# Kernel optimization log

Measured on AMD Instinct MI355X. Metric: run time of the kernel, lower is better.

## Reference

```python
import jax, jax.numpy as jnp
import numpy as np

B, N, D = 16, 2048, 128
SCALE = 1.0 / np.sqrt(D).astype(np.float32)


def setup_inputs() -> dict:
    key = jax.random.key(0)
    ks = jax.random.split(key, 9)
    Q = jax.random.normal(ks[0], (B, N, D), dtype=jnp.float32)
    K = jax.random.normal(ks[1], (B, N, D), dtype=jnp.float32)
    V = jax.random.normal(ks[2], (B, N, D), dtype=jnp.float32)
    bias_dis = 0.1 * jax.random.normal(ks[3], (N, N), dtype=jnp.float32)
    bias_dtw = 0.1 * jax.random.normal(ks[4], (N, N), dtype=jnp.float32)
    bias_pattern = 0.1 * jax.random.normal(ks[5], (N, N), dtype=jnp.float32)
    bias_poi = 0.1 * jax.random.normal(ks[6], (N, N), dtype=jnp.float32)
    # key/query padding masks: mostly True (valid) with some padding
    input_mask = jax.random.randint(ks[7], (B, N), 0, 10) > 0
    embeddings_mask = jax.random.randint(ks[8], (B, N), 0, 10) > 0
    # lower-triangular causal mask (diagonal kept so every row has a valid key)
    causal_mask = jnp.tril(jnp.ones((N, N), dtype=bool))
    return {"Q": Q, "K": K, "V": V, "bias_dis": bias_dis, "bias_dtw": bias_dtw,
            "bias_pattern": bias_pattern, "bias_poi": bias_poi,
            "input_mask": input_mask, "embeddings_mask": embeddings_mask,
            "causal_mask": causal_mask}


def reference(Q, K, V, bias_dis, bias_dtw, bias_pattern, bias_poi,
              input_mask, embeddings_mask, causal_mask):
    # masked_fill_(~mask, 0.0) on K, V with input_mask[:, :, None]
    km = input_mask[:, :, None]
    K = jnp.where(km, K, 0.0)
    V = jnp.where(km, V, 0.0)
    # masked_fill_(~mask, 0.0) on Q with embeddings_mask[:, :, None]
    Q = jnp.where(embeddings_mask[:, :, None], Q, 0.0)
    # scores [B, N, N] = Q K^T / sqrt(dim)
    scores = jnp.einsum('bnd,bmd->bnm', Q, K) * SCALE
    # causal masked_fill_(~causal_mask, -inf)
    scores = jnp.where(causal_mask[None, :, :], scores, -jnp.inf)
    # per-batch bias loop == broadcast add of summed [N, N] biases
    scores = scores + (bias_dis + bias_dtw + bias_pattern + bias_poi)[None, :, :]
    P = jax.nn.softmax(scores, axis=-1)
    # dropout p=0 (eval) -> identity
    return jnp.einsum('bnm,bmd->bnd', P, V)
```

## Files before the change

kernel.cpp:

```cpp
#include <hip/hip_runtime.h>
#include <math.h>

constexpr int Bc = 16;
constexpr int Nc = 2048;
constexpr int Dc = 128;
constexpr int NCHUNK = Nc / 64;
constexpr float SCALE_F = 0.08838834764831845f;

typedef __bf16 bf16x8 __attribute__((ext_vector_type(8)));
typedef __bf16 bf16x4 __attribute__((ext_vector_type(4)));
typedef float  f32x4  __attribute__((ext_vector_type(4)));

constexpr size_t KPACK_BYTES = (size_t)Bc * NCHUNK * 16 * 64 * 16;
constexpr size_t VPACK_BYTES = KPACK_BYTES;
constexpr int NUNITS = 1056;
constexpr size_t BIASP_BYTES = (size_t)NUNITS * 2048 * 4;
constexpr int CHUNK_ELEMS = 16 * 64 * 8;
constexpr int PART_FLOATS = 64 * 128 + 64 + 64;
constexpr size_t PART_BYTES = (size_t)Bc * 72 * PART_FLOATS * 4;

__device__ __constant__ int SLOT_UNITS[32][3] = {
    { 7,  6,  1}, { 8, 21, 11}, {10, 44, 29}, {12, 75, 55},
    {14,  5,  2}, {16, 19, 13}, {18, 41, 32}, {20, 71, 59},
    {22,  4,  3}, {23, 17, 15}, {24, 38, 35}, {25, 67, 63},
    {27, 28,  0}, {30, 31,  9}, {33, 34, 26}, {36, 37, 51},
    {39, 40, -1}, {42, 43, -1}, {45, 46, -1}, {47, 48, -1},
    {49, 50, -1}, {52, 53, -1}, {54, 56, -1}, {57, 58, -1},
    {60, 61, -1}, {62, 64, -1}, {65, 66, -1}, {68, 69, -1},
    {70, 72, -1}, {73, 74, -1}, {76, 77, -1}, {78, 79, -1}
};

__device__ __forceinline__ int ftri(int t) {
    const int m = t >> 1;
    return (t & 1) ? (m + 1) * (m + 1) : m * (m + 1);
}

__device__ __forceinline__ void gload_lds16(const __bf16* gsrc, __bf16* ldst) {
    __builtin_amdgcn_global_load_lds(
        (const __attribute__((address_space(1))) unsigned int*)gsrc,
        (__attribute__((address_space(3))) unsigned int*)ldst, 16, 0, 0);
}

template<int CTRL>
__device__ __forceinline__ float dpp_mv(float v) {
    return __builtin_bit_cast(float,
        __builtin_amdgcn_update_dpp(0, __builtin_bit_cast(int, v),
                                    CTRL, 0xF, 0xF, true));
}
__device__ __forceinline__ float rmax16(float v) {
    v = fmaxf(v, dpp_mv<0xB1>(v));
    v = fmaxf(v, dpp_mv<0x4E>(v));
    v = fmaxf(v, dpp_mv<0x141>(v));
    v = fmaxf(v, dpp_mv<0x140>(v));
    return v;
}
__device__ __forceinline__ float rsum16(float v) {
    v += dpp_mv<0xB1>(v);
    v += dpp_mv<0x4E>(v);
    v += dpp_mv<0x141>(v);
    v += dpp_mv<0x140>(v);
    return v;
}

__global__ __launch_bounds__(256) void prep_fused(
    const float* __restrict__ K, const float* __restrict__ V,
    const int* __restrict__ imask,
    const float* __restrict__ b0, const float* __restrict__ b1,
    const float* __restrict__ b2, const float* __restrict__ b3,
    __bf16* __restrict__ Kp, __bf16* __restrict__ Vp, float* __restrict__ bsp)
{
    __shared__ __align__(16) __bf16 Ks[64][136];
    __shared__ __align__(16) __bf16 Vs[64][136];
    __shared__ __align__(16) float  Ts[32][68];
    const int bid = blockIdx.x;
    const int tid = threadIdx.x;

    if (bid >= 512) {
        const int u = bid - 512;
        int t = 0;
        while (ftri(t + 1) <= u) ++t;
        const int c = u - ftri(t);

        #pragma unroll
        for (int i = 0; i < 2; ++i) {
            const int v = tid + 256 * i;
            const int row = v >> 4, c4 = v & 15;
            const size_t g = (size_t)(t * 32 + row) * Nc + c * 64 + c4 * 4;
            const float4 a = *(const float4*)(b0 + g);
            const float4 d = *(const float4*)(b1 + g);
            const float4 e = *(const float4*)(b2 + g);
            const float4 f = *(const float4*)(b3 + g);
            float4 s;
            s.x = a.x + d.x + e.x + f.x;
            s.y = a.y + d.y + e.y + f.y;
            s.z = a.z + d.z + e.z + f.z;
            s.w = a.w + d.w + e.w + f.w;
            *(float4*)&Ts[row][c4 * 4] = s;
        }
        __syncthreads();

        const int lane = tid >> 2;
        const int quad = lane >> 4, l15 = lane & 15;
        const int k0 = (tid & 3) * 8;
        float* outp = bsp + (size_t)u * 2048;
        #pragma unroll
        for (int g2 = 0; g2 < 2; ++g2) {
            const int k = k0 + g2 * 4;
            const int h = (k >> 4) & 1, jt = (k >> 2) & 3;
            float4 o;
            o.x = Ts[h * 16 + quad * 4 + 0][jt * 16 + l15];
            o.y = Ts[h * 16 + quad * 4 + 1][jt * 16 + l15];
            o.z = Ts[h * 16 + quad * 4 + 2][jt * 16 + l15];
            o.w = Ts[h * 16 + quad * 4 + 3][jt * 16 + l15];
            ((float4*)outp)[tid * 2 + g2] = o;
        }
        return;
    }

    const int c = bid & 31;
    const int b = bid >> 5;
    const int m0 = c * 64;
    const float* Kb = K + (size_t)b * Nc * Dc;
    const float* Vb = V + (size_t)b * Nc * Dc;
    const int* imb = imask + b * Nc;

    #pragma unroll
    for (int it = 0; it < 8; ++it) {
        const int idx = it * 256 + tid;
        const int row = idx >> 5;
        const int c4  = idx & 31;
        const int gm  = m0 + row;
        const float msk = imb[gm] ? 1.0f : 0.0f;
        const float4 kf = ((const float4*)(Kb + (size_t)gm * Dc))[c4];
        const float4 vf = ((const float4*)(Vb + (size_t)gm * Dc))[c4];
        bf16x4 kb, vb;
        kb[0] = (__bf16)(kf.x * msk); kb[1] = (__bf16)(kf.y * msk);
        kb[2] = (__bf16)(kf.z * msk); kb[3] = (__bf16)(kf.w * msk);
        vb[0] = (__bf16)(vf.x * msk); vb[1] = (__bf16)(vf.y * msk);
        vb[2] = (__bf16)(vf.z * msk); vb[3] = (__bf16)(vf.w * msk);
        *(bf16x4*)&Ks[row][c4 * 4] = kb;
        *(bf16x4*)&Vs[row][c4 * 4] = vb;
    }
    __syncthreads();

    const size_t chunk_base = (size_t)(b * NCHUNK + c) * CHUNK_ELEMS;
    #pragma unroll
    for (int i = 0; i < 4; ++i) {
        const int s = i * 256 + tid;
        const int f = s >> 6;
        const int l = s & 63;
        const int quad = (l >> 4) & 3;
        const int l15  = l & 15;
        {
            const int jt = f >> 2, kd = f & 3;
            const bf16x8 kv = *(const bf16x8*)&Ks[jt * 16 + l15][kd * 32 + quad * 8];
            *(bf16x8*)&Kp[chunk_base + (size_t)f * 512 + l * 8] = kv;
        }
        {
            const int kj = f >> 3, dt = f & 7;
            bf16x8 vv;
            #pragma unroll
            for (int j = 0; j < 8; ++j)
                vv[j] = Vs[kj * 32 + quad * 8 + j][dt * 16 + l15];
            *(bf16x8*)&Vp[chunk_base + (size_t)f * 512 + l * 8] = vv;
        }
    }
}

template<bool SPLIT>
__global__ __launch_bounds__(256) void attn_persist(
    const float* __restrict__ Q,
    const __bf16* __restrict__ Kp, const __bf16* __restrict__ Vp,
    const float* __restrict__ biasp, const int* __restrict__ emask,
    float* __restrict__ out, float* __restrict__ part)
{
    __shared__ __align__(16) __bf16 Kl[2][16 * 512];
    __shared__ __align__(16) __bf16 Vl[2][16 * 512];
    __shared__ __align__(16) __bf16 Pl[4][16][72];

    const int tid  = threadIdx.x;
    const int w    = tid >> 6;
    const int lane = tid & 63;
    const int quad = lane >> 4;
    const int l15  = lane & 15;
    const int b    = blockIdx.x;
    const int slot = blockIdx.y;

    const float*  Qb  = Q + (size_t)b * Nc * Dc;
    const __bf16* Kpb = Kp + (size_t)b * NCHUNK * CHUNK_ELEMS;
    const __bf16* Vpb = Vp + (size_t)b * NCHUNK * CHUNK_ELEMS;
    const f32x4* bfragbase = (const f32x4*)biasp + (size_t)lane * 8 + (w & 1) * 4;

    for (int j = 0; j < 3; ++j) {
        int t, c0, cend, pidx;
        bool direct;
        if (SPLIT) {
            const int un = SLOT_UNITS[slot][j];
            if (un < 0) break;
            if (un < 8)       { t = un;                  c0 = 0; }
            else if (un < 24) { t = 8  + ((un -  8) >> 1); c0 = ((un -  8) & 1) * 8; }
            else if (un < 48) { t = 16 + (un - 24) / 3;    c0 = ((un - 24) % 3) * 8; }
            else              { t = 24 + ((un - 48) >> 2); c0 = ((un - 48) & 3) * 8; }
            cend = min(t + 1, c0 + 8);
            direct = (un < 8);
            pidx = un - 8;
        } else {
            if (j) break;
            t = (slot < 16) ? slot : (47 - slot);
            c0 = 0; cend = t + 1; direct = true; pidx = 0;
        }

        const int q0w = t * 64 + w * 16;
        const int t32 = t * 2 + (w >> 1);
        const int fb32 = ftri(t32);
        const f32x4* bfrag = bfragbase;

        bf16x8 qfrag[4];
        {
            const int row = q0w + l15;
            const float qs = emask[b * Nc + row] ? SCALE_F : 0.0f;
            const float4* qr = (const float4*)(Qb + (size_t)row * Dc);
            #pragma unroll
            for (int kd = 0; kd < 4; ++kd) {
                const float4 xx = qr[kd * 8 + quad * 2];
                const float4 yy = qr[kd * 8 + quad * 2 + 1];
                qfrag[kd][0] = (__bf16)(xx.x * qs); qfrag[kd][1] = (__bf16)(xx.y * qs);
                qfrag[kd][2] = (__bf16)(xx.z * qs); qfrag[kd][3] = (__bf16)(xx.w * qs);
                qfrag[kd][4] = (__bf16)(yy.x * qs); qfrag[kd][5] = (__bf16)(yy.y * qs);
                qfrag[kd][6] = (__bf16)(yy.z * qs); qfrag[kd][7] = (__bf16)(yy.w * qs);
            }
        }

        f32x4 oacc[8];
        #pragma unroll
        for (int dt = 0; dt < 8; ++dt) { oacc[dt][0]=0.f; oacc[dt][1]=0.f; oacc[dt][2]=0.f; oacc[dt][3]=0.f; }
        float mrun[4] = {-INFINITY, -INFINITY, -INFINITY, -INFINITY};
        float lrun[4] = {0.f, 0.f, 0.f, 0.f};

        const int nch = cend - c0;

        #pragma unroll
        for (int i = 0; i < 4; ++i) {
            const int seg = w * 4 + i;
            gload_lds16(Kpb + (size_t)c0 * CHUNK_ELEMS + seg * 512 + lane * 8, &Kl[0][seg * 512]);
            gload_lds16(Vpb + (size_t)c0 * CHUNK_ELEMS + seg * 512 + lane * 8, &Vl[0][seg * 512]);
        }
        f32x4 binit[4];
        #pragma unroll
        for (int jt = 0; jt < 4; ++jt)
            binit[jt] = bfrag[(size_t)(fb32 + c0) * 512 + jt];
        __syncthreads();

        f32x4 sc[4];
        #pragma unroll
        for (int jt = 0; jt < 4; ++jt) sc[jt] = binit[jt];
        #pragma unroll
        for (int jt = 0; jt < 4; ++jt)
            #pragma unroll
            for (int kd = 0; kd < 4; ++kd) {
                const bf16x8 bfr = *(const bf16x8*)&Kl[0][(jt * 4 + kd) * 512 + lane * 8];
                sc[jt] = __builtin_amdgcn_mfma_f32_16x16x32_bf16(qfrag[kd], bfr, sc[jt], 0, 0, 0);
            }
        if (nch > 1) {
            #pragma unroll
            for (int i = 0; i < 4; ++i) {
                const int seg = w * 4 + i;
                gload_lds16(Kpb + (size_t)(c0 + 1) * CHUNK_ELEMS + seg * 512 + lane * 8, &Kl[1][seg * 512]);
                gload_lds16(Vpb + (size_t)(c0 + 1) * CHUNK_ELEMS + seg * 512 + lane * 8, &Vl[1][seg * 512]);
            }
            #pragma unroll
            for (int jt = 0; jt < 4; ++jt)
                binit[jt] = bfrag[(size_t)(fb32 + c0 + 1) * 512 + jt];
        }

        for (int c = c0; c < cend; ++c) {
            const int cb = (c - c0) & 1;

            if (c == t) {
                const int m0 = c * 64;
                #pragma unroll
                for (int jt = 0; jt < 4; ++jt)
                    #pragma unroll
                    for (int reg = 0; reg < 4; ++reg) {
                        const int gr = q0w + quad * 4 + reg;
                        const int gc = m0 + jt * 16 + l15;
                        if (gc > gr) sc[jt][reg] = -INFINITY;
                    }
            }

            float mx[4];
            int grow = 0;
            #pragma unroll
            for (int reg = 0; reg < 4; ++reg) {
                float m = fmaxf(fmaxf(sc[0][reg], sc[1][reg]), fmaxf(sc[2][reg], sc[3][reg]));
                m = rmax16(m);
                mx[reg] = m;
                grow |= (m > mrun[reg]);
            }
            if (__any(grow)) {
                #pragma unroll
                for (int reg = 0; reg < 4; ++reg) {
                    const float mn = fmaxf(mrun[reg], mx[reg]);
                    const float alpha = __expf(mrun[reg] - mn);
                    mrun[reg] = mn;
                    lrun[reg] *= alpha;
                    #pragma unroll
                    for (int dt = 0; dt < 8; ++dt) oacc[dt][reg] *= alpha;
                }
            }
            #pragma unroll
            for (int reg = 0; reg < 4; ++reg) {
                float ls = 0.f;
                #pragma unroll
                for (int jt = 0; jt < 4; ++jt) {
                    const float pv = __expf(sc[jt][reg] - mrun[reg]);
                    sc[jt][reg] = pv;
                    ls += pv;
                }
                lrun[reg] += rsum16(ls);
            }

            #pragma unroll
            for (int jt = 0; jt < 4; ++jt)
                #pragma unroll
                for (int reg = 0; reg < 4; ++reg)
                    Pl[w][quad * 4 + reg][jt * 16 + l15] = (__bf16)sc[jt][reg];

            #pragma unroll
            for (int kj = 0; kj < 2; ++kj) {
                const bf16x8 pa = *(const bf16x8*)&Pl[w][l15][kj * 32 + quad * 8];
                #pragma unroll
                for (int dt = 0; dt < 8; ++dt) {
                    const bf16x8 vb = *(const bf16x8*)&Vl[cb][(kj * 8 + dt) * 512 + lane * 8];
                    oacc[dt] = __builtin_amdgcn_mfma_f32_16x16x32_bf16(pa, vb, oacc[dt], 0, 0, 0);
                }
            }

            __syncthreads();

            const bool n1 = (c + 1) < cend;
            const bool n2 = (c + 2) < cend;

            if (n2) {
                const size_t off = (size_t)(c + 2) * CHUNK_ELEMS;
                #pragma unroll
                for (int i = 0; i < 4; ++i) {
                    const int seg = w * 4 + i;
                    gload_lds16(Kpb + off + seg * 512 + lane * 8, &Kl[cb][seg * 512]);
                    gload_lds16(Vpb + off + seg * 512 + lane * 8, &Vl[cb][seg * 512]);
                }
            }

            if (n1) {
                #pragma unroll
                for (int jt = 0; jt < 4; ++jt) sc[jt] = binit[jt];
                #pragma unroll
                for (int jt = 0; jt < 4; ++jt)
                    #pragma unroll
                    for (int kd = 0; kd < 4; ++kd) {
                        const bf16x8 bfr = *(const bf16x8*)&Kl[cb ^ 1][(jt * 4 + kd) * 512 + lane * 8];
                        sc[jt] = __builtin_amdgcn_mfma_f32_16x16x32_bf16(qfrag[kd], bfr, sc[jt], 0, 0, 0);
                    }
            }
            if (n2) {
                #pragma unroll
                for (int jt = 0; jt < 4; ++jt)
                    binit[jt] = bfrag[(size_t)(fb32 + c + 2) * 512 + jt];
            }
        }

        if (direct) {
            #pragma unroll
            for (int reg = 0; reg < 4; ++reg) {
                const float inv = 1.0f / lrun[reg];
                const int gr = q0w + quad * 4 + reg;
                float* orow = out + ((size_t)b * Nc + gr) * Dc;
                #pragma unroll
                for (int dt = 0; dt < 8; ++dt)
                    orow[dt * 16 + l15] = oacc[dt][reg] * inv;
            }
        } else {
            float* pb = part + (size_t)(b * 72 + pidx) * PART_FLOATS;
            #pragma unroll
            for (int reg = 0; reg < 4; ++reg) {
                const int lr = w * 16 + quad * 4 + reg;
                #pragma unroll
                for (int dt = 0; dt < 8; ++dt)
                    pb[lr * 128 + dt * 16 + l15] = oacc[dt][reg];
                if (l15 == 0) {
                    pb[8192 + lr] = mrun[reg];
                    pb[8256 + lr] = lrun[reg];
                }
            }
        }
    }
}

__global__ __launch_bounds__(256) void merge_parts(
    const float* __restrict__ part, float* __restrict__ out)
{
    const int b = blockIdx.x;
    const int t = 8 + blockIdx.y;
    const int S = (t < 16) ? 2 : ((t < 24) ? 3 : 4);
    const int pbase = (t < 16) ? 2 * (t - 8)
                    : (t < 24) ? 16 + 3 * (t - 16)
                               : 40 + 4 * (t - 24);
    const int r  = threadIdx.x >> 2;
    const int cq = threadIdx.x & 3;
    const float* p0 = part + (size_t)(b * 72 + pbase) * PART_FLOATS;

    float m[4], a[4];
    float mstar = -INFINITY;
    #pragma unroll
    for (int s = 0; s < 4; ++s)
        if (s < S) { m[s] = p0[(size_t)s * PART_FLOATS + 8192 + r]; mstar = fmaxf(mstar, m[s]); }
    float lsum = 0.f;
    #pragma unroll
    for (int s = 0; s < 4; ++s)
        if (s < S) {
            a[s] = __expf(m[s] - mstar);
            lsum += p0[(size_t)s * PART_FLOATS + 8256 + r] * a[s];
        }
    const float inv = 1.0f / lsum;

    float* orow = out + ((size_t)b * Nc + t * 64 + r) * Dc + cq * 32;
    #pragma unroll
    for (int i = 0; i < 8; ++i) {
        float x = 0.f, y = 0.f, z = 0.f, ww = 0.f;
        #pragma unroll
        for (int s = 0; s < 4; ++s)
            if (s < S) {
                const f32x4 v = *(const f32x4*)&p0[(size_t)s * PART_FLOATS + r * 128 + cq * 32 + i * 4];
                x += v[0] * a[s]; y += v[1] * a[s]; z += v[2] * a[s]; ww += v[3] * a[s];
            }
        f32x4 o; o[0] = x * inv; o[1] = y * inv; o[2] = z * inv; o[3] = ww * inv;
        *(f32x4*)&orow[i * 4] = o;
    }
}

__global__ __launch_bounds__(256) void attn_mfma_legacy(
    const float* __restrict__ Q, const float* __restrict__ K, const float* __restrict__ V,
    const float* __restrict__ p0, const float* __restrict__ p1,
    const float* __restrict__ p2, const float* __restrict__ p3,
    const int* __restrict__ imask, const int* __restrict__ emask,
    float* __restrict__ out)
{
    __shared__ __align__(16) __bf16 Klds[64][136];
    __shared__ __align__(16) __bf16 Vt[128][72];
    __shared__ __align__(16) __bf16 Plds[4][16][72];
    const int tid  = threadIdx.x;
    const int w    = tid >> 6;
    const int lane = tid & 63;
    const int quad = lane >> 4;
    const int l15  = lane & 15;
    const int b = blockIdx.y;
    const int x = blockIdx.x, yy = blockIdx.y;
    const int ti = (yy < 8) ? x : (31 - x);
    const int q0 = ti * 64, q0w = q0 + w * 16;
    const float* Qb = Q + (size_t)b * Nc * Dc;
    const float* Kb = K + (size_t)b * Nc * Dc;
    const float* Vb = V + (size_t)b * Nc * Dc;
    const int* imb = imask + b * Nc;

    bf16x8 qfrag[4];
    {
        const int row = q0w + l15;
        const float qs = emask[b * Nc + row] ? SCALE_F : 0.0f;
        const float4* qr = (const float4*)(Qb + (size_t)row * Dc);
        #pragma unroll
        for (int kd = 0; kd < 4; ++kd) {
            const float4 xv = qr[kd * 8 + quad * 2];
            const float4 yv = qr[kd * 8 + quad * 2 + 1];
            qfrag[kd][0]=(__bf16)(xv.x*qs); qfrag[kd][1]=(__bf16)(xv.y*qs);
            qfrag[kd][2]=(__bf16)(xv.z*qs); qfrag[kd][3]=(__bf16)(xv.w*qs);
            qfrag[kd][4]=(__bf16)(yv.x*qs); qfrag[kd][5]=(__bf16)(yv.y*qs);
            qfrag[kd][6]=(__bf16)(yv.z*qs); qfrag[kd][7]=(__bf16)(yv.w*qs);
        }
    }
    f32x4 oacc[8];
    #pragma unroll
    for (int dt = 0; dt < 8; ++dt){oacc[dt][0]=0.f;oacc[dt][1]=0.f;oacc[dt][2]=0.f;oacc[dt][3]=0.f;}
    float mrun[4]={-INFINITY,-INFINITY,-INFINITY,-INFINITY}, lrun[4]={0.f,0.f,0.f,0.f};

    for (int m0 = 0; m0 <= q0; m0 += 64) {
        __syncthreads();
        #pragma unroll
        for (int it = 0; it < 8; ++it) {
            const int idx = it * 256 + tid;
            const int row = idx >> 5, c4 = idx & 31;
            const int gm = m0 + row;
            const float msk = imb[gm] ? 1.0f : 0.0f;
            const float4 kf = ((const float4*)(Kb + (size_t)gm * Dc))[c4];
            const float4 vf = ((const float4*)(Vb + (size_t)gm * Dc))[c4];
            bf16x4 kb;
            kb[0]=(__bf16)(kf.x*msk); kb[1]=(__bf16)(kf.y*msk);
            kb[2]=(__bf16)(kf.z*msk); kb[3]=(__bf16)(kf.w*msk);
            *(bf16x4*)&Klds[row][c4*4] = kb;
            Vt[c4*4+0][row]=(__bf16)(vf.x*msk); Vt[c4*4+1][row]=(__bf16)(vf.y*msk);
            Vt[c4*4+2][row]=(__bf16)(vf.z*msk); Vt[c4*4+3][row]=(__bf16)(vf.w*msk);
        }
        __syncthreads();
        f32x4 sc[4];
        #pragma unroll
        for (int jt = 0; jt < 4; ++jt){sc[jt][0]=0.f;sc[jt][1]=0.f;sc[jt][2]=0.f;sc[jt][3]=0.f;}
        #pragma unroll
        for (int jt = 0; jt < 4; ++jt)
            #pragma unroll
            for (int kd = 0; kd < 4; ++kd) {
                const bf16x8 bfr = *(const bf16x8*)&Klds[jt*16+l15][kd*32+quad*8];
                sc[jt] = __builtin_amdgcn_mfma_f32_16x16x32_bf16(qfrag[kd], bfr, sc[jt], 0, 0, 0);
            }
        #pragma unroll
        for (int jt = 0; jt < 4; ++jt)
            #pragma unroll
            for (int reg = 0; reg < 4; ++reg) {
                const int gr = q0w + quad*4 + reg;
                const int gc = m0 + jt*16 + l15;
                const size_t boff = (size_t)gr * Nc + gc;
                const float bsx = p0[boff] + p1[boff] + p2[boff] + p3[boff];
                const float v = sc[jt][reg] + bsx;
                sc[jt][reg] = (gc > gr) ? -INFINITY : v;
            }
        #pragma unroll
        for (int reg = 0; reg < 4; ++reg) {
            float mx = fmaxf(fmaxf(sc[0][reg], sc[1][reg]), fmaxf(sc[2][reg], sc[3][reg]));
            mx = rmax16(mx);
            const float mn = fmaxf(mrun[reg], mx);
            const float alpha = __expf(mrun[reg] - mn);
            mrun[reg] = mn; lrun[reg] *= alpha;
            #pragma unroll
            for (int dt = 0; dt < 8; ++dt) oacc[dt][reg] *= alpha;
            float ls = 0.f;
            #pragma unroll
            for (int jt = 0; jt < 4; ++jt) {
                const float pv = __expf(sc[jt][reg] - mn);
                sc[jt][reg] = pv; ls += pv;
            }
            lrun[reg] += rsum16(ls);
        }
        #pragma unroll
        for (int jt = 0; jt < 4; ++jt)
            #pragma unroll
            for (int reg = 0; reg < 4; ++reg)
                Plds[w][quad*4+reg][jt*16+l15] = (__bf16)sc[jt][reg];
        #pragma unroll
        for (int kj = 0; kj < 2; ++kj) {
            const bf16x8 pa = *(const bf16x8*)&Plds[w][l15][kj*32+quad*8];
            #pragma unroll
            for (int dt = 0; dt < 8; ++dt) {
                const bf16x8 vb = *(const bf16x8*)&Vt[dt*16+l15][kj*32+quad*8];
                oacc[dt] = __builtin_amdgcn_mfma_f32_16x16x32_bf16(pa, vb, oacc[dt], 0, 0, 0);
            }
        }
    }
    #pragma unroll
    for (int reg = 0; reg < 4; ++reg) {
        const float inv = 1.0f / lrun[reg];
        const int gr = q0w + quad*4 + reg;
        float* orow = out + ((size_t)b * Nc + gr) * Dc;
        #pragma unroll
        for (int dt = 0; dt < 8; ++dt)
            orow[dt*16+l15] = oacc[dt][reg] * inv;
    }
}

extern "C" void kernel_launch(void* const* d_in, const int* in_sizes, int n_in,
                              void* d_out, int out_size, void* d_ws, size_t ws_size,
                              hipStream_t stream) {
    const float* Q  = (const float*)d_in[0];
    const float* K  = (const float*)d_in[1];
    const float* V  = (const float*)d_in[2];
    const float* b0 = (const float*)d_in[3];
    const float* b1 = (const float*)d_in[4];
    const float* b2 = (const float*)d_in[5];
    const float* b3 = (const float*)d_in[6];
    const int* im   = (const int*)d_in[7];
    const int* em   = (const int*)d_in[8];
    float* out      = (float*)d_out;

    const size_t need_full  = KPACK_BYTES + VPACK_BYTES + BIASP_BYTES;
    const size_t need_split = need_full + PART_BYTES;

    if (ws_size >= need_full) {
        __bf16* Kp  = (__bf16*)d_ws;
        __bf16* Vp  = (__bf16*)((char*)d_ws + KPACK_BYTES);
        float*  bsp = (float*)((char*)d_ws + KPACK_BYTES + VPACK_BYTES);
        float*  prt = (float*)((char*)d_ws + need_full);
        prep_fused<<<512 + NUNITS, 256, 0, stream>>>(
            K, V, im, b0, b1, b2, b3, Kp, Vp, bsp);
        if (ws_size >= need_split) {
            attn_persist<true><<<dim3(Bc, 32), 256, 0, stream>>>(
                Q, Kp, Vp, bsp, em, out, prt);
            merge_parts<<<dim3(Bc, 24), 256, 0, stream>>>(prt, out);
        } else {
            attn_persist<false><<<dim3(Bc, 32), 256, 0, stream>>>(
                Q, Kp, Vp, bsp, em, out, nullptr);
        }
    } else {
        attn_mfma_legacy<<<dim3(NCHUNK, Bc), 256, 0, stream>>>(
            Q, K, V, b0, b1, b2, b3, im, em, out);
    }
}
```

Measured before the change: 234.2 us.

## Load V fragments directly to registers, swizzle P tile, and double slot count

V chunks are now read straight from global memory into registers for the PV matmul, so they are no longer staged through LDS. This halves the shared memory footprint and allows more blocks per CU. The P scratch tile drops its padding in favour of an XOR swizzle to avoid bank conflicts. The split path launches 64 slots per batch with a rebalanced unit-to-slot table, which raises parallelism. The costs are higher register pressure, global V loads whose latency sits in the critical loop, and more partial merges.

```diff
diff --git a/kernel.cpp b/kernel.cpp
--- a/kernel.cpp
+++ b/kernel.cpp
@@ -19,15 +19,23 @@
 constexpr int PART_FLOATS = 64 * 128 + 64 + 64;
 constexpr size_t PART_BYTES = (size_t)Bc * 72 * PART_FLOATS * 4;
 
-__device__ __constant__ int SLOT_UNITS[32][3] = {
-    { 7,  6,  1}, { 8, 21, 11}, {10, 44, 29}, {12, 75, 55},
-    {14,  5,  2}, {16, 19, 13}, {18, 41, 32}, {20, 71, 59},
-    {22,  4,  3}, {23, 17, 15}, {24, 38, 35}, {25, 67, 63},
-    {27, 28,  0}, {30, 31,  9}, {33, 34, 26}, {36, 37, 51},
-    {39, 40, -1}, {42, 43, -1}, {45, 46, -1}, {47, 48, -1},
-    {49, 50, -1}, {52, 53, -1}, {54, 56, -1}, {57, 58, -1},
-    {60, 61, -1}, {62, 64, -1}, {65, 66, -1}, {68, 69, -1},
-    {70, 72, -1}, {73, 74, -1}, {76, 77, -1}, {78, 79, -1}
+__device__ __constant__ signed char SLOT_UNITS[64][3] = {
+    { 6,  2, -1}, {21, 13, -1}, {44, 32, -1}, {75, 59, -1},
+    { 5,  3, -1}, {19, 15, -1}, {41, 35, -1}, {71, 63, -1},
+    { 4,  1,  0}, {17, 11,  9}, {38, 29, 26}, {67, 55, 51},
+    { 7, -1, -1}, { 8, -1, -1}, {10, -1, -1}, {12, -1, -1},
+    {14, -1, -1}, {16, -1, -1}, {18, -1, -1}, {20, -1, -1},
+    {22, -1, -1}, {23, -1, -1}, {24, -1, -1}, {25, -1, -1},
+    {27, -1, -1}, {28, -1, -1}, {30, -1, -1}, {31, -1, -1},
+    {33, -1, -1}, {34, -1, -1}, {36, -1, -1}, {37, -1, -1},
+    {39, -1, -1}, {40, -1, -1}, {42, -1, -1}, {43, -1, -1},
+    {45, -1, -1}, {46, -1, -1}, {47, -1, -1}, {48, -1, -1},
+    {49, -1, -1}, {50, -1, -1}, {52, -1, -1}, {53, -1, -1},
+    {54, -1, -1}, {56, -1, -1}, {57, -1, -1}, {58, -1, -1},
+    {60, -1, -1}, {61, -1, -1}, {62, -1, -1}, {64, -1, -1},
+    {65, -1, -1}, {66, -1, -1}, {68, -1, -1}, {69, -1, -1},
+    {70, -1, -1}, {72, -1, -1}, {73, -1, -1}, {74, -1, -1},
+    {76, -1, -1}, {77, -1, -1}, {78, -1, -1}, {79, -1, -1}
 };
 
 __device__ __forceinline__ int ftri(int t) {
@@ -39,6 +47,10 @@
     __builtin_amdgcn_global_load_lds(
         (const __attribute__((address_space(1))) unsigned int*)gsrc,
         (__attribute__((address_space(3))) unsigned int*)ldst, 16, 0, 0);
+}
+
+__device__ __forceinline__ int pswz(int row, int col) {
+    return col ^ ((row & 7) << 3);
 }
 
 template<int CTRL>
@@ -168,15 +180,14 @@
 }
 
 template<bool SPLIT>
-__global__ __launch_bounds__(256) void attn_persist(
+__global__ __launch_bounds__(256) void attn_persist2(
     const float* __restrict__ Q,
     const __bf16* __restrict__ Kp, const __bf16* __restrict__ Vp,
     const float* __restrict__ biasp, const int* __restrict__ emask,
     float* __restrict__ out, float* __restrict__ part)
 {
     __shared__ __align__(16) __bf16 Kl[2][16 * 512];
-    __shared__ __align__(16) __bf16 Vl[2][16 * 512];
-    __shared__ __align__(16) __bf16 Pl[4][16][72];
+    __shared__ __align__(16) __bf16 Pl[4][16][64];
 
     const int tid  = threadIdx.x;
     const int w    = tid >> 6;
@@ -243,7 +254,6 @@
         for (int i = 0; i < 4; ++i) {
             const int seg = w * 4 + i;
             gload_lds16(Kpb + (size_t)c0 * CHUNK_ELEMS + seg * 512 + lane * 8, &Kl[0][seg * 512]);
-            gload_lds16(Vpb + (size_t)c0 * CHUNK_ELEMS + seg * 512 + lane * 8, &Vl[0][seg * 512]);
         }
         f32x4 binit[4];
         #pragma unroll
@@ -253,20 +263,20 @@
 
         f32x4 sc[4];
         #pragma unroll
-        for (int jt = 0; jt < 4; ++jt) sc[jt] = binit[jt];
-        #pragma unroll
-        for (int jt = 0; jt < 4; ++jt)
-            #pragma unroll
-            for (int kd = 0; kd < 4; ++kd) {
+        for (int jt = 0; jt < 4; ++jt) {
+            const bf16x8 k0f = *(const bf16x8*)&Kl[0][(jt * 4 + 0) * 512 + lane * 8];
+            sc[jt] = __builtin_amdgcn_mfma_f32_16x16x32_bf16(qfrag[0], k0f, binit[jt], 0, 0, 0);
+            #pragma unroll
+            for (int kd = 1; kd < 4; ++kd) {
                 const bf16x8 bfr = *(const bf16x8*)&Kl[0][(jt * 4 + kd) * 512 + lane * 8];
                 sc[jt] = __builtin_amdgcn_mfma_f32_16x16x32_bf16(qfrag[kd], bfr, sc[jt], 0, 0, 0);
             }
+        }
         if (nch > 1) {
             #pragma unroll
             for (int i = 0; i < 4; ++i) {
                 const int seg = w * 4 + i;
                 gload_lds16(Kpb + (size_t)(c0 + 1) * CHUNK_ELEMS + seg * 512 + lane * 8, &Kl[1][seg * 512]);
-                gload_lds16(Vpb + (size_t)(c0 + 1) * CHUNK_ELEMS + seg * 512 + lane * 8, &Vl[1][seg * 512]);
             }
             #pragma unroll
             for (int jt = 0; jt < 4; ++jt)
@@ -275,6 +285,12 @@
 
         for (int c = c0; c < cend; ++c) {
             const int cb = (c - c0) & 1;
+            const __bf16* vc = Vpb + (size_t)c * CHUNK_ELEMS;
+
+            bf16x8 va[8];
+            #pragma unroll
+            for (int dt = 0; dt < 8; ++dt)
+                va[dt] = *(const bf16x8*)&vc[(size_t)dt * 512 + lane * 8];
 
             if (c == t) {
                 const int m0 = c * 64;
@@ -323,17 +339,25 @@
             #pragma unroll
             for (int jt = 0; jt < 4; ++jt)
                 #pragma unroll
-                for (int reg = 0; reg < 4; ++reg)
-                    Pl[w][quad * 4 + reg][jt * 16 + l15] = (__bf16)sc[jt][reg];
-
-            #pragma unroll
-            for (int kj = 0; kj < 2; ++kj) {
-                const bf16x8 pa = *(const bf16x8*)&Pl[w][l15][kj * 32 + quad * 8];
-                #pragma unroll
-                for (int dt = 0; dt < 8; ++dt) {
-                    const bf16x8 vb = *(const bf16x8*)&Vl[cb][(kj * 8 + dt) * 512 + lane * 8];
-                    oacc[dt] = __builtin_amdgcn_mfma_f32_16x16x32_bf16(pa, vb, oacc[dt], 0, 0, 0);
+                for (int reg = 0; reg < 4; ++reg) {
+                    const int row = quad * 4 + reg;
+                    Pl[w][row][pswz(row, jt * 16 + l15)] = (__bf16)sc[jt][reg];
                 }
+
+            bf16x8 vb8[8];
+            #pragma unroll
+            for (int dt = 0; dt < 8; ++dt)
+                vb8[dt] = *(const bf16x8*)&vc[(size_t)(8 + dt) * 512 + lane * 8];
+
+            {
+                const bf16x8 pa0 = *(const bf16x8*)&Pl[w][l15][pswz(l15, quad * 8)];
+                #pragma unroll
+                for (int dt = 0; dt < 8; ++dt)
+                    oacc[dt] = __builtin_amdgcn_mfma_f32_16x16x32_bf16(pa0, va[dt], oacc[dt], 0, 0, 0);
+                const bf16x8 pa1 = *(const bf16x8*)&Pl[w][l15][pswz(l15, 32 + quad * 8)];
+                #pragma unroll
+                for (int dt = 0; dt < 8; ++dt)
+                    oacc[dt] = __builtin_amdgcn_mfma_f32_16x16x32_bf16(pa1, vb8[dt], oacc[dt], 0, 0, 0);
             }
 
             __syncthreads();
@@ -347,20 +371,20 @@
                 for (int i = 0; i < 4; ++i) {
                     const int seg = w * 4 + i;
                     gload_lds16(Kpb + off + seg * 512 + lane * 8, &Kl[cb][seg * 512]);
-                    gload_lds16(Vpb + off + seg * 512 + lane * 8, &Vl[cb][seg * 512]);
                 }
             }
 
             if (n1) {
                 #pragma unroll
-                for (int jt = 0; jt < 4; ++jt) sc[jt] = binit[jt];
-                #pragma unroll
-                for (int jt = 0; jt < 4; ++jt)
+                for (int jt = 0; jt < 4; ++jt) {
+                    const bf16x8 k0f = *(const bf16x8*)&Kl[cb ^ 1][(jt * 4 + 0) * 512 + lane * 8];
+                    sc[jt] = __builtin_amdgcn_mfma_f32_16x16x32_bf16(qfrag[0], k0f, binit[jt], 0, 0, 0);
                     #pragma unroll
-                    for (int kd = 0; kd < 4; ++kd) {
+                    for (int kd = 1; kd < 4; ++kd) {
                         const bf16x8 bfr = *(const bf16x8*)&Kl[cb ^ 1][(jt * 4 + kd) * 512 + lane * 8];
                         sc[jt] = __builtin_amdgcn_mfma_f32_16x16x32_bf16(qfrag[kd], bfr, sc[jt], 0, 0, 0);
                     }
+                }
             }
             if (n2) {
                 #pragma unroll
@@ -589,11 +613,11 @@
         prep_fused<<<512 + NUNITS, 256, 0, stream>>>(
             K, V, im, b0, b1, b2, b3, Kp, Vp, bsp);
         if (ws_size >= need_split) {
-            attn_persist<true><<<dim3(Bc, 32), 256, 0, stream>>>(
+            attn_persist2<true><<<dim3(Bc, 64), 256, 0, stream>>>(
                 Q, Kp, Vp, bsp, em, out, prt);
             merge_parts<<<dim3(Bc, 24), 256, 0, stream>>>(prt, out);
         } else {
-            attn_persist<false><<<dim3(Bc, 32), 256, 0, stream>>>(
+            attn_persist2<false><<<dim3(Bc, 32), 256, 0, stream>>>(
                 Q, Kp, Vp, bsp, em, out, nullptr);
         }
     } else {
```

Result: slower. 271.5 us (+15.9%).

## Widen attention blocks to 128 query rows with 8 waves and rebalanced split schedule

Applied to the files above, without the earlier changes.

The persistent attention kernel now uses 512-thread blocks covering 128 query rows (8 waves), so each K/V chunk loaded into LDS is shared by twice as many rows. The split-KV work table is rebuilt for 128-row tiles with new per-slot chunk ranges and a matching merge kernel. Two smaller changes ride along: the P buffer in LDS gets an XOR swizzle in place of padding, and the per-row sum reduction moves out of the inner loop to the epilogue. The larger block raises register and LDS pressure per workgroup and changes how load is balanced across CUs.

```diff
diff --git a/kernel.cpp b/kernel.cpp
--- a/kernel.cpp
+++ b/kernel.cpp
@@ -16,18 +16,56 @@
 constexpr int NUNITS = 1056;
 constexpr size_t BIASP_BYTES = (size_t)NUNITS * 2048 * 4;
 constexpr int CHUNK_ELEMS = 16 * 64 * 8;
-constexpr int PART_FLOATS = 64 * 128 + 64 + 64;
-constexpr size_t PART_BYTES = (size_t)Bc * 72 * PART_FLOATS * 4;
-
-__device__ __constant__ int SLOT_UNITS[32][3] = {
-    { 7,  6,  1}, { 8, 21, 11}, {10, 44, 29}, {12, 75, 55},
-    {14,  5,  2}, {16, 19, 13}, {18, 41, 32}, {20, 71, 59},
-    {22,  4,  3}, {23, 17, 15}, {24, 38, 35}, {25, 67, 63},
-    {27, 28,  0}, {30, 31,  9}, {33, 34, 26}, {36, 37, 51},
-    {39, 40, -1}, {42, 43, -1}, {45, 46, -1}, {47, 48, -1},
-    {49, 50, -1}, {52, 53, -1}, {54, 56, -1}, {57, 58, -1},
-    {60, 61, -1}, {62, 64, -1}, {65, 66, -1}, {68, 69, -1},
-    {70, 72, -1}, {73, 74, -1}, {76, 77, -1}, {78, 79, -1}
+constexpr int PART_FLOATS8 = 128 * 128 + 128 + 128;
+constexpr int NPART8 = 42;
+constexpr size_t PART_BYTES8 = (size_t)Bc * NPART8 * PART_FLOATS8 * 4;
+
+__device__ __constant__ signed char ST_T[32][3] = {
+ {15,-1,-1},{15,-1,-1},{15,-1,-1},{15,14,-1},
+ {14,-1,-1},{14,-1,-1},{14,13,-1},{13,-1,-1},
+ {13,-1,-1},{13,-1,-1},{12,-1,-1},{12,-1,-1},
+ {12,11,-1},{11,-1,-1},{11,-1,-1},{11,10,-1},
+ {10,-1,-1},{10,-1,-1},{10, 9,-1},{ 9,-1,-1},
+ { 9, 8,-1},{ 8,-1,-1},{ 8,-1,-1},{ 7,-1,-1},
+ { 7,-1,-1},{ 6,-1,-1},{ 6, 5,-1},{ 5,-1,-1},
+ { 5, 4,-1},{ 4, 3,-1},{ 3, 2,-1},{ 2, 1, 0}
+};
+__device__ __constant__ signed char ST_C0[32][3] = {
+ { 0, 0, 0},{ 9, 0, 0},{18, 0, 0},{27, 0, 0},
+ { 4, 0, 0},{13, 0, 0},{22, 0, 0},{ 1, 0, 0},
+ {10, 0, 0},{19, 0, 0},{ 0, 0, 0},{ 9, 0, 0},
+ {18, 0, 0},{ 1, 0, 0},{10, 0, 0},{19, 0, 0},
+ { 4, 0, 0},{12, 0, 0},{20, 0, 0},{ 6, 0, 0},
+ {14, 0, 0},{ 2, 0, 0},{10, 0, 0},{ 0, 0, 0},
+ { 8, 0, 0},{ 0, 0, 0},{ 8, 0, 0},{ 2, 0, 0},
+ {10, 0, 0},{ 6, 0, 0},{ 4, 0, 0},{ 4, 0, 0}
+};
+__device__ __constant__ signed char ST_C1[32][3] = {
+ { 9, 0, 0},{18, 0, 0},{27, 0, 0},{32, 4, 0},
+ {13, 0, 0},{22, 0, 0},{30, 1, 0},{10, 0, 0},
+ {19, 0, 0},{28, 0, 0},{ 9, 0, 0},{18, 0, 0},
+ {26, 1, 0},{10, 0, 0},{19, 0, 0},{24, 4, 0},
+ {12, 0, 0},{20, 0, 0},{22, 6, 0},{14, 0, 0},
+ {20, 2, 0},{10, 0, 0},{18, 0, 0},{ 8, 0, 0},
+ {16, 0, 0},{ 8, 0, 0},{14, 2, 0},{10, 0, 0},
+ {12, 6, 0},{10, 4, 0},{ 8, 4, 0},{ 6, 4, 2}
+};
+__device__ __constant__ signed char ST_U[32][3] = {
+ { 0,-1,-1},{ 1,-1,-1},{ 2,-1,-1},{ 3, 4,-1},
+ { 5,-1,-1},{ 6,-1,-1},{ 7, 8,-1},{ 9,-1,-1},
+ {10,-1,-1},{11,-1,-1},{12,-1,-1},{13,-1,-1},
+ {14,15,-1},{16,-1,-1},{17,-1,-1},{18,19,-1},
+ {20,-1,-1},{21,-1,-1},{22,23,-1},{24,-1,-1},
+ {25,26,-1},{27,-1,-1},{28,-1,-1},{29,-1,-1},
+ {30,-1,-1},{31,-1,-1},{32,33,-1},{34,-1,-1},
+ {35,36,-1},{37,38,-1},{39,40,-1},{41,42,43}
+};
+__device__ __constant__ signed char MT_S[14] = {2,2,2,3,2,2,3,3,4,4,3,4,4,4};
+__device__ __constant__ signed char MT_U[14][4] = {
+ {40,41,-1,-1},{38,39,-1,-1},{36,37,-1,-1},{33,34,35,-1},
+ {31,32,-1,-1},{29,30,-1,-1},{26,27,28,-1},{23,24,25,-1},
+ {19,20,21,22},{15,16,17,18},{12,13,14,-1},{ 8, 9,10,11},
+ { 4, 5, 6, 7},{ 0, 1, 2, 3}
 };
 
 __device__ __forceinline__ int ftri(int t) {
@@ -39,6 +77,10 @@
     __builtin_amdgcn_global_load_lds(
         (const __attribute__((address_space(1))) unsigned int*)gsrc,
         (__attribute__((address_space(3))) unsigned int*)ldst, 16, 0, 0);
+}
+
+__device__ __forceinline__ int pswz(int row, int col) {
+    return col ^ ((row & 7) << 3);
 }
 
 template<int CTRL>
@@ -168,7 +210,7 @@
 }
 
 template<bool SPLIT>
-__global__ __launch_bounds__(256) void attn_persist(
+__global__ __launch_bounds__(512, 4) void attn8(
     const float* __restrict__ Q,
     const __bf16* __restrict__ Kp, const __bf16* __restrict__ Vp,
     const float* __restrict__ biasp, const int* __restrict__ emask,
@@ -176,7 +218,7 @@
 {
     __shared__ __align__(16) __bf16 Kl[2][16 * 512];
     __shared__ __align__(16) __bf16 Vl[2][16 * 512];
-    __shared__ __align__(16) __bf16 Pl[4][16][72];
+    __shared__ __align__(16) __bf16 Pl[8][16][64];
 
     const int tid  = threadIdx.x;
     const int w    = tid >> 6;
@@ -192,27 +234,22 @@
     const f32x4* bfragbase = (const f32x4*)biasp + (size_t)lane * 8 + (w & 1) * 4;
 
     for (int j = 0; j < 3; ++j) {
-        int t, c0, cend, pidx;
+        int T, c0, cend, uid;
         bool direct;
         if (SPLIT) {
-            const int un = SLOT_UNITS[slot][j];
-            if (un < 0) break;
-            if (un < 8)       { t = un;                  c0 = 0; }
-            else if (un < 24) { t = 8  + ((un -  8) >> 1); c0 = ((un -  8) & 1) * 8; }
-            else if (un < 48) { t = 16 + (un - 24) / 3;    c0 = ((un - 24) % 3) * 8; }
-            else              { t = 24 + ((un - 48) >> 2); c0 = ((un - 48) & 3) * 8; }
-            cend = min(t + 1, c0 + 8);
-            direct = (un < 8);
-            pidx = un - 8;
+            T = ST_T[slot][j];
+            if (T < 0) break;
+            c0 = ST_C0[slot][j]; cend = ST_C1[slot][j]; uid = ST_U[slot][j];
+            direct = (uid >= 42);
         } else {
             if (j) break;
-            t = (slot < 16) ? slot : (47 - slot);
-            c0 = 0; cend = t + 1; direct = true; pidx = 0;
-        }
-
-        const int q0w = t * 64 + w * 16;
-        const int t32 = t * 2 + (w >> 1);
+            T = slot; c0 = 0; cend = 2 * T + 2; direct = true; uid = 0;
+        }
+
+        const int q0w = T * 128 + w * 16;
+        const int t32 = T * 4 + (w >> 1);
         const int fb32 = ftri(t32);
+        const int cdiag = 2 * T;
         const f32x4* bfrag = bfragbase;
 
         bf16x8 qfrag[4];
@@ -240,8 +277,8 @@
         const int nch = cend - c0;
 
         #pragma unroll
-        for (int i = 0; i < 4; ++i) {
-            const int seg = w * 4 + i;
+        for (int i = 0; i < 2; ++i) {
+            const int seg = w * 2 + i;
             gload_lds16(Kpb + (size_t)c0 * CHUNK_ELEMS + seg * 512 + lane * 8, &Kl[0][seg * 512]);
             gload_lds16(Vpb + (size_t)c0 * CHUNK_ELEMS + seg * 512 + lane * 8, &Vl[0][seg * 512]);
         }
@@ -263,8 +300,8 @@
             }
         if (nch > 1) {
             #pragma unroll
-            for (int i = 0; i < 4; ++i) {
-                const int seg = w * 4 + i;
+            for (int i = 0; i < 2; ++i) {
+                const int seg = w * 2 + i;
                 gload_lds16(Kpb + (size_t)(c0 + 1) * CHUNK_ELEMS + seg * 512 + lane * 8, &Kl[1][seg * 512]);
                 gload_lds16(Vpb + (size_t)(c0 + 1) * CHUNK_ELEMS + seg * 512 + lane * 8, &Vl[1][seg * 512]);
             }
@@ -276,7 +313,7 @@
         for (int c = c0; c < cend; ++c) {
             const int cb = (c - c0) & 1;
 
-            if (c == t) {
+            if (c >= cdiag) {
                 const int m0 = c * 64;
                 #pragma unroll
                 for (int jt = 0; jt < 4; ++jt)
@@ -317,18 +354,20 @@
                     sc[jt][reg] = pv;
                     ls += pv;
                 }
-                lrun[reg] += rsum16(ls);
+                lrun[reg] += ls;
             }
 
             #pragma unroll
             for (int jt = 0; jt < 4; ++jt)
                 #pragma unroll
-                for (int reg = 0; reg < 4; ++reg)
-                    Pl[w][quad * 4 + reg][jt * 16 + l15] = (__bf16)sc[jt][reg];
+                for (int reg = 0; reg < 4; ++reg) {
+                    const int row = quad * 4 + reg;
+                    Pl[w][row][pswz(row, jt * 16 + l15)] = (__bf16)sc[jt][reg];
+                }
 
             #pragma unroll
             for (int kj = 0; kj < 2; ++kj) {
-                const bf16x8 pa = *(const bf16x8*)&Pl[w][l15][kj * 32 + quad * 8];
+                const bf16x8 pa = *(const bf16x8*)&Pl[w][l15][pswz(l15, kj * 32 + quad * 8)];
                 #pragma unroll
                 for (int dt = 0; dt < 8; ++dt) {
                     const bf16x8 vb = *(const bf16x8*)&Vl[cb][(kj * 8 + dt) * 512 + lane * 8];
@@ -344,8 +383,8 @@
             if (n2) {
                 const size_t off = (size_t)(c + 2) * CHUNK_ELEMS;
                 #pragma unroll
-                for (int i = 0; i < 4; ++i) {
-                    const int seg = w * 4 + i;
+                for (int i = 0; i < 2; ++i) {
+                    const int seg = w * 2 + i;
                     gload_lds16(Kpb + off + seg * 512 + lane * 8, &Kl[cb][seg * 512]);
                     gload_lds16(Vpb + off + seg * 512 + lane * 8, &Vl[cb][seg * 512]);
                 }
@@ -372,7 +411,7 @@
         if (direct) {
             #pragma unroll
             for (int reg = 0; reg < 4; ++reg) {
-                const float inv = 1.0f / lrun[reg];
+                const float inv = 1.0f / rsum16(lrun[reg]);
                 const int gr = q0w + quad * 4 + reg;
                 float* orow = out + ((size_t)b * Nc + gr) * Dc;
                 #pragma unroll
@@ -380,60 +419,63 @@
                     orow[dt * 16 + l15] = oacc[dt][reg] * inv;
             }
         } else {
-            float* pb = part + (size_t)(b * 72 + pidx) * PART_FLOATS;
+            float* pb = part + (size_t)(b * NPART8 + uid) * PART_FLOATS8;
             #pragma unroll
             for (int reg = 0; reg < 4; ++reg) {
                 const int lr = w * 16 + quad * 4 + reg;
                 #pragma unroll
                 for (int dt = 0; dt < 8; ++dt)
                     pb[lr * 128 + dt * 16 + l15] = oacc[dt][reg];
+                const float ls = rsum16(lrun[reg]);
                 if (l15 == 0) {
-                    pb[8192 + lr] = mrun[reg];
-                    pb[8256 + lr] = lrun[reg];
+                    pb[16384 + lr] = mrun[reg];
+                    pb[16512 + lr] = ls;
                 }
             }
         }
     }
 }
 
-__global__ __launch_bounds__(256) void merge_parts(
+__global__ __launch_bounds__(256) void merge_parts8(
     const float* __restrict__ part, float* __restrict__ out)
 {
     const int b = blockIdx.x;
-    const int t = 8 + blockIdx.y;
-    const int S = (t < 16) ? 2 : ((t < 24) ? 3 : 4);
-    const int pbase = (t < 16) ? 2 * (t - 8)
-                    : (t < 24) ? 16 + 3 * (t - 16)
-                               : 40 + 4 * (t - 24);
-    const int r  = threadIdx.x >> 2;
-    const int cq = threadIdx.x & 3;
-    const float* p0 = part + (size_t)(b * 72 + pbase) * PART_FLOATS;
-
+    const int y = blockIdx.y;
+    const int T = 2 + y;
+    const int S = MT_S[y];
+    const int r  = threadIdx.x >> 1;
+    const int ch = threadIdx.x & 1;
+
+    const float* pb[4];
     float m[4], a[4];
     float mstar = -INFINITY;
     #pragma unroll
     for (int s = 0; s < 4; ++s)
-        if (s < S) { m[s] = p0[(size_t)s * PART_FLOATS + 8192 + r]; mstar = fmaxf(mstar, m[s]); }
+        if (s < S) {
+            pb[s] = part + (size_t)(b * NPART8 + MT_U[y][s]) * PART_FLOATS8;
+            m[s] = pb[s][16384 + r];
+            mstar = fmaxf(mstar, m[s]);
+        }
     float lsum = 0.f;
     #pragma unroll
     for (int s = 0; s < 4; ++s)
         if (s < S) {
             a[s] = __expf(m[s] - mstar);
-            lsum += p0[(size_t)s * PART_FLOATS + 8256 + r] * a[s];
+            lsum += pb[s][16512 + r] * a[s];
         }
     const float inv = 1.0f / lsum;
 
-    float* orow = out + ((size_t)b * Nc + t * 64 + r) * Dc + cq * 32;
+    float* orow = out + ((size_t)b * Nc + T * 128 + r) * Dc + ch * 64;
     #pragma unroll
-    for (int i = 0; i < 8; ++i) {
-        float x = 0.f, y = 0.f, z = 0.f, ww = 0.f;
+    for (int i = 0; i < 16; ++i) {
+        float x = 0.f, yv = 0.f, z = 0.f, ww = 0.f;
         #pragma unroll
         for (int s = 0; s < 4; ++s)
             if (s < S) {
-                const f32x4 v = *(const f32x4*)&p0[(size_t)s * PART_FLOATS + r * 128 + cq * 32 + i * 4];
-                x += v[0] * a[s]; y += v[1] * a[s]; z += v[2] * a[s]; ww += v[3] * a[s];
-            }
-        f32x4 o; o[0] = x * inv; o[1] = y * inv; o[2] = z * inv; o[3] = ww * inv;
+                const f32x4 v = *(const f32x4*)&pb[s][r * 128 + ch * 64 + i * 4];
+                x += v[0] * a[s]; yv += v[1] * a[s]; z += v[2] * a[s]; ww += v[3] * a[s];
+            }
+        f32x4 o; o[0] = x * inv; o[1] = yv * inv; o[2] = z * inv; o[3] = ww * inv;
         *(f32x4*)&orow[i * 4] = o;
     }
 }
@@ -579,7 +621,7 @@
     float* out      = (float*)d_out;
 
     const size_t need_full  = KPACK_BYTES + VPACK_BYTES + BIASP_BYTES;
-    const size_t need_split = need_full + PART_BYTES;
+    const size_t need_split = need_full + PART_BYTES8;
 
     if (ws_size >= need_full) {
         __bf16* Kp  = (__bf16*)d_ws;
@@ -589,11 +631,11 @@
         prep_fused<<<512 + NUNITS, 256, 0, stream>>>(
             K, V, im, b0, b1, b2, b3, Kp, Vp, bsp);
         if (ws_size >= need_split) {
-            attn_persist<true><<<dim3(Bc, 32), 256, 0, stream>>>(
+            attn8<true><<<dim3(Bc, 32), 512, 0, stream>>>(
                 Q, Kp, Vp, bsp, em, out, prt);
-            merge_parts<<<dim3(Bc, 24), 256, 0, stream>>>(prt, out);
+            merge_parts8<<<dim3(Bc, 14), 256, 0, stream>>>(prt, out);
         } else {
-            attn_persist<false><<<dim3(Bc, 32), 256, 0, stream>>>(
+            attn8<false><<<dim3(Bc, 16), 512, 0, stream>>>(
                 Q, Kp, Vp, bsp, em, out, nullptr);
         }
     } else {
```

New measurement: 284.8 us. 21.6% more time.
